# Kernel tuning notes

Hardware: AMD Instinct MI355X
Metric: run time of the kernel (lower is better)

## Reference

```python
import jax, jax.numpy as jnp
import numpy as np

N, NPER, B, E = 65536, 1024, 64, 1048576
IN_F, HID, K, NCLS = 128, 64, 16, 10


def setup_inputs() -> dict:
    key = jax.random.key(0)
    ks = jax.random.split(key, 12)
    x = jax.random.normal(ks[0], (N, IN_F), jnp.float32)
    # block-structured intra-graph edges: 64 graphs of 1024 contiguous nodes
    gid = jax.random.randint(ks[1], (E,), 0, B)
    src = gid * NPER + jax.random.randint(ks[2], (E,), 0, NPER)
    dst = gid * NPER + jax.random.randint(ks[3], (E,), 0, NPER)
    edge_index = jnp.stack([src, dst]).astype(jnp.int32)
    batch = (jnp.arange(N, dtype=jnp.int32) // NPER).astype(jnp.int32)
    def lin(k, fo, fi):
        kw, kb = jax.random.split(k)
        s = 1.0 / np.sqrt(fi)
        return (jax.random.uniform(kw, (fo, fi), jnp.float32, -s, s),
                jax.random.uniform(kb, (fo,), jnp.float32, -s, s))
    W1, b1 = lin(ks[4], HID, IN_F)
    W2, b2 = lin(ks[5], HID, HID)
    Wp, bp = lin(ks[6], K, HID)      # DMoN cluster-assignment MLP (single Linear)
    Wl, bl = lin(ks[7], NCLS, HID)   # final classifier
    return {"x": x, "edge_index": edge_index, "batch": batch,
            "W1": W1, "b1": b1, "W2": W2, "b2": b2,
            "Wp": Wp, "bp": bp, "Wl": Wl, "bl": bl}


def gcn_conv(x, src, dst, W, b):
    # GCNConv with add_self_loops=True, symmetric normalization
    n = x.shape[0]
    deg = jax.ops.segment_sum(jnp.ones(src.shape[0], x.dtype), dst,
                              num_segments=n) + 1.0  # +1 for self-loop
    dinv = jax.lax.rsqrt(deg)
    h = x @ W.T
    coef = (dinv[src] * dinv[dst])[:, None]
    agg = jax.ops.segment_sum(h[src] * coef, dst, num_segments=n)
    agg = agg + h * (dinv * dinv)[:, None]  # self-loop contribution
    return agg + b


def reference(x, edge_index, batch, W1, b1, W2, b2, Wp, bp, Wl, bl):
    src, dst = edge_index[0], edge_index[1]
    h = jax.nn.relu(gcn_conv(x, src, dst, W1, b1))
    h = jax.nn.relu(gcn_conv(h, src, dst, W2, b2))
    # to_dense_batch: graphs are equal-sized and contiguous -> reshape, mask all True
    Xb = h.reshape(B, NPER, HID)
    # DMoN cluster assignment (dropout=0.0, mask all ones)
    s = jax.nn.softmax(Xb @ Wp.T + bp, axis=-1)          # [B, NPER, K]
    Xp = jax.nn.selu(jnp.einsum('bnk,bnh->bkh', s, Xb))   # pooled clusters [B, K, HID]
    out = Xp.mean(axis=1)                                  # [B, HID]
    logits = out @ Wl.T + bl                               # [B, NCLS]
    return logits
```

## Files before the change

kernel.cpp:

```cpp
#include <hip/hip_runtime.h>
#include <cstddef>

#define N_NODES 65536
#define NPER    1024
#define NGRAPH  64
#define HID     64
#define IN_F    128
#define KCLUS   16
#define NCLS    10
#define ECAP    20480
#define HSTRIDE 12
#define ZROW    NPER

__global__ __launch_bounds__(256) void bucket_kernel(const int* __restrict__ src,
                                                     const int* __restrict__ dst,
                                                     int* __restrict__ ecnt,
                                                     int* __restrict__ gedges, int E) {
    __shared__ int hist[NGRAPH];
    __shared__ int base_l[NGRAPH];
    const int t = threadIdx.x;
    const int e0 = blockIdx.x * 1024;
    if (t < NGRAPH) hist[t] = 0;
    __syncthreads();

    int gg[4], rr[4], pk[4];
#pragma unroll
    for (int i = 0; i < 4; ++i) {
        int idx = e0 + i * 256 + t;
        if (idx < E) {
            int d = dst[idx], s = src[idx];
            int g = d >> 10;
            gg[i] = g;
            pk[i] = ((d & 1023) << 10) | (s & 1023);
            rr[i] = atomicAdd(&hist[g], 1);
        } else gg[i] = -1;
    }
    __syncthreads();
    if (t < NGRAPH) base_l[t] = atomicAdd(&ecnt[t], hist[t]);
    __syncthreads();
#pragma unroll
    for (int i = 0; i < 4; ++i) {
        if (gg[i] >= 0) {
            int pos = base_l[gg[i]] + rr[i];
            if (pos < ECAP) gedges[gg[i] * ECAP + pos] = pk[i];
        }
    }
}

__global__ __launch_bounds__(1024) void csr_kernel(const int* __restrict__ gedges,
                                                   const int* __restrict__ ecnt,
                                                   int* __restrict__ rp,
                                                   unsigned short* __restrict__ esorted,
                                                   float* __restrict__ dinv) {
    __shared__ int hist[NPER];
    __shared__ int wsum[16];
    const int g = blockIdx.x, t = threadIdx.x;
    const int lane = t & 63, wid = t >> 6;
    const int ec = ecnt[g];
    const int* ge = gedges + (size_t)g * ECAP;

    hist[t] = 0;
    __syncthreads();
    for (int i = t; i < ec; i += 1024) atomicAdd(&hist[ge[i] >> 10], 1);
    __syncthreads();

    const int h0 = hist[t];
    const int pd = (h0 + 3) & ~3;
    int v = pd;
#pragma unroll
    for (int off = 1; off < 64; off <<= 1) {
        int x = __shfl_up(v, off, 64);
        if (lane >= off) v += x;
    }
    if (lane == 63) wsum[wid] = v;
    __syncthreads();
    if (wid == 0) {
        int wv = (lane < 16) ? wsum[lane] : 0;
#pragma unroll
        for (int off = 1; off < 16; off <<= 1) {
            int x = __shfl_up(wv, off, 64);
            if (lane >= off) wv += x;
        }
        if (lane < 16) wsum[lane] = wv;
    }
    __syncthreads();
    const int incl = v + (wid > 0 ? wsum[wid - 1] : 0);
    const int excl = incl - pd;

    rp[g * (NPER + 1) + t] = excl;
    if (t == NPER - 1) rp[g * (NPER + 1) + NPER] = incl;
    dinv[g * NPER + t] = rsqrtf((float)h0 + 1.0f);

    hist[t] = excl;
    __syncthreads();

    unsigned short* es = esorted + (size_t)g * ECAP;
    for (int i = t; i < ec; i += 1024) {
        int pk = ge[i];
        int pos = atomicAdd(&hist[pk >> 10], 1);
        es[pos] = (unsigned short)(pk & 1023);
    }
    __syncthreads();
    for (int q = excl + h0; q < excl + pd; ++q) es[q] = (unsigned short)ZROW;
}

template <int K>
__global__ __launch_bounds__(256) void linear_kernel(const float* __restrict__ X,
                                                     const float* __restrict__ W,
                                                     float* __restrict__ Y) {
    __shared__ float xsT[64][68];
    __shared__ float wsT[64][68];
    const int t = threadIdx.x;
    const size_t row0 = (size_t)blockIdx.x * 64;
    const int r0 = (t >> 4) * 4;
    const int c0 = (t & 15) * 4;
    float acc[4][4] = {};

    for (int kc = 0; kc < K; kc += 64) {
        __syncthreads();
        for (int i = t; i < 1024; i += 256) {
            int row = i >> 4, k4 = (i & 15) << 2;
            float4 v = *(const float4*)(X + (row0 + row) * K + kc + k4);
            xsT[k4 + 0][row] = v.x;
            xsT[k4 + 1][row] = v.y;
            xsT[k4 + 2][row] = v.z;
            xsT[k4 + 3][row] = v.w;
        }
        for (int i = t; i < 1024; i += 256) {
            int col = i >> 4, k4 = (i & 15) << 2;
            float4 v = *(const float4*)(W + col * K + kc + k4);
            wsT[k4 + 0][col] = v.x;
            wsT[k4 + 1][col] = v.y;
            wsT[k4 + 2][col] = v.z;
            wsT[k4 + 3][col] = v.w;
        }
        __syncthreads();

#pragma unroll 8
        for (int k = 0; k < 64; ++k) {
            float4 xv = *(const float4*)&xsT[k][r0];
            float4 wv = *(const float4*)&wsT[k][c0];
            acc[0][0] = fmaf(xv.x, wv.x, acc[0][0]);
            acc[0][1] = fmaf(xv.x, wv.y, acc[0][1]);
            acc[0][2] = fmaf(xv.x, wv.z, acc[0][2]);
            acc[0][3] = fmaf(xv.x, wv.w, acc[0][3]);
            acc[1][0] = fmaf(xv.y, wv.x, acc[1][0]);
            acc[1][1] = fmaf(xv.y, wv.y, acc[1][1]);
            acc[1][2] = fmaf(xv.y, wv.z, acc[1][2]);
            acc[1][3] = fmaf(xv.y, wv.w, acc[1][3]);
            acc[2][0] = fmaf(xv.z, wv.x, acc[2][0]);
            acc[2][1] = fmaf(xv.z, wv.y, acc[2][1]);
            acc[2][2] = fmaf(xv.z, wv.z, acc[2][2]);
            acc[2][3] = fmaf(xv.z, wv.w, acc[2][3]);
            acc[3][0] = fmaf(xv.w, wv.x, acc[3][0]);
            acc[3][1] = fmaf(xv.w, wv.y, acc[3][1]);
            acc[3][2] = fmaf(xv.w, wv.z, acc[3][2]);
            acc[3][3] = fmaf(xv.w, wv.w, acc[3][3]);
        }
    }

#pragma unroll
    for (int i = 0; i < 4; ++i) {
        float4 v = make_float4(acc[i][0], acc[i][1], acc[i][2], acc[i][3]);
        *(float4*)(Y + (row0 + r0 + i) * HID + c0) = v;
    }
}

__global__ __launch_bounds__(512) void agg_kernel(const float* __restrict__ h,
                                                  const unsigned short* __restrict__ esorted,
                                                  const int* __restrict__ rp,
                                                  const float* __restrict__ dinv,
                                                  const float* __restrict__ bias,
                                                  float* __restrict__ outp) {
    __shared__ float Hs[(NPER + 1) * HSTRIDE];
    __shared__ float dl[NPER];
    const int g = blockIdx.x & 63;
    const int f0 = (blockIdx.x >> 6) * 8;
    const int t = threadIdx.x;
    const int base = g * NPER;

    for (int r = t; r < NPER; r += 512) {
        const float* hp = h + (size_t)(base + r) * HID + f0;
        float4 a = *(const float4*)hp;
        float4 b = *(const float4*)(hp + 4);
        float dv = dinv[base + r];
        dl[r] = dv;
        float* row = &Hs[r * HSTRIDE];
        *(float4*)row = make_float4(a.x * dv, a.y * dv, a.z * dv, a.w * dv);
        *(float4*)(row + 4) = make_float4(b.x * dv, b.y * dv, b.z * dv, b.w * dv);
    }
    if (t < HSTRIDE) Hs[ZROW * HSTRIDE + t] = 0.f;
    float bb[8];
#pragma unroll
    for (int j = 0; j < 8; ++j) bb[j] = bias[f0 + j];
    const unsigned short* es = esorted + (size_t)g * ECAP;
    const int* rpg = rp + g * (NPER + 1);
    __syncthreads();

    for (int ld = t; ld < NPER; ld += 512) {
        int p = rpg[ld];
        const int pe = rpg[ld + 1];
        const float* srow = &Hs[ld * HSTRIDE];
        float4 acc0 = *(const float4*)srow;
        float4 acc1 = *(const float4*)(srow + 4);
        float4 bcc0 = make_float4(0.f, 0.f, 0.f, 0.f);
        float4 bcc1 = make_float4(0.f, 0.f, 0.f, 0.f);

        for (; p < pe; p += 4) {
            uint2 w4 = *(const uint2*)(es + p);
            const float* r0 = &Hs[(int)(w4.x & 0xFFFFu) * HSTRIDE];
            const float* r1 = &Hs[(int)(w4.x >> 16) * HSTRIDE];
            const float* r2 = &Hs[(int)(w4.y & 0xFFFFu) * HSTRIDE];
            const float* r3 = &Hs[(int)(w4.y >> 16) * HSTRIDE];
            float4 a0 = *(const float4*)r0, a1 = *(const float4*)(r0 + 4);
            float4 b0 = *(const float4*)r1, b1 = *(const float4*)(r1 + 4);
            float4 c0v = *(const float4*)r2, c1v = *(const float4*)(r2 + 4);
            float4 d0 = *(const float4*)r3, d1 = *(const float4*)(r3 + 4);
            acc0.x += a0.x; acc0.y += a0.y; acc0.z += a0.z; acc0.w += a0.w;
            acc1.x += a1.x; acc1.y += a1.y; acc1.z += a1.z; acc1.w += a1.w;
            bcc0.x += b0.x; bcc0.y += b0.y; bcc0.z += b0.z; bcc0.w += b0.w;
            bcc1.x += b1.x; bcc1.y += b1.y; bcc1.z += b1.z; bcc1.w += b1.w;
            acc0.x += c0v.x; acc0.y += c0v.y; acc0.z += c0v.z; acc0.w += c0v.w;
            acc1.x += c1v.x; acc1.y += c1v.y; acc1.z += c1v.z; acc1.w += c1v.w;
            bcc0.x += d0.x; bcc0.y += d0.y; bcc0.z += d0.z; bcc0.w += d0.w;
            bcc1.x += d1.x; bcc1.y += d1.y; bcc1.z += d1.z; bcc1.w += d1.w;
        }
        acc0.x += bcc0.x; acc0.y += bcc0.y; acc0.z += bcc0.z; acc0.w += bcc0.w;
        acc1.x += bcc1.x; acc1.y += bcc1.y; acc1.z += bcc1.z; acc1.w += bcc1.w;

        const float dv = dl[ld];
        float4 o0, o1;
        o0.x = fmaxf(fmaf(acc0.x, dv, bb[0]), 0.f);
        o0.y = fmaxf(fmaf(acc0.y, dv, bb[1]), 0.f);
        o0.z = fmaxf(fmaf(acc0.z, dv, bb[2]), 0.f);
        o0.w = fmaxf(fmaf(acc0.w, dv, bb[3]), 0.f);
        o1.x = fmaxf(fmaf(acc1.x, dv, bb[4]), 0.f);
        o1.y = fmaxf(fmaf(acc1.y, dv, bb[5]), 0.f);
        o1.z = fmaxf(fmaf(acc1.z, dv, bb[6]), 0.f);
        o1.w = fmaxf(fmaf(acc1.w, dv, bb[7]), 0.f);
        float* op = outp + (size_t)(base + ld) * HID + f0;
        *(float4*)op = o0;
        *(float4*)(op + 4) = o1;
    }
}

__global__ __launch_bounds__(256) void pool1_kernel(const float* __restrict__ h,
                                                    const float* __restrict__ Wp,
                                                    const float* __restrict__ bp,
                                                    float* __restrict__ xpart) {
    __shared__ float xs[128][HID + 1];
    __shared__ float ss[128][KCLUS + 1];
    __shared__ float wp[KCLUS][HID];
    __shared__ float bps[KCLUS];
    const int g = blockIdx.x >> 3;
    const int c = blockIdx.x & 7;
    const int t = threadIdx.x;
    const float* hb = h + ((size_t)g * NPER + c * 128) * HID;

    for (int i = t; i < 128 * HID / 4; i += 256) {
        float4 v = ((const float4*)hb)[i];
        int row = i >> 4, col = (i & 15) * 4;
        xs[row][col] = v.x; xs[row][col + 1] = v.y; xs[row][col + 2] = v.z; xs[row][col + 3] = v.w;
    }
    for (int i = t; i < KCLUS * HID; i += 256) wp[i >> 6][i & 63] = Wp[i];
    if (t < KCLUS) bps[t] = bp[t];
    __syncthreads();

    if (t < 128) {
        float lg[KCLUS];
        float mx = -1e30f;
#pragma unroll
        for (int k = 0; k < KCLUS; ++k) {
            float a = bps[k];
#pragma unroll 8
            for (int hh = 0; hh < HID; ++hh) a = fmaf(xs[t][hh], wp[k][hh], a);
            lg[k] = a;
            mx = fmaxf(mx, a);
        }
        float sum = 0.f;
#pragma unroll
        for (int k = 0; k < KCLUS; ++k) {
            lg[k] = __expf(lg[k] - mx);
            sum += lg[k];
        }
        float inv = 1.0f / sum;
#pragma unroll
        for (int k = 0; k < KCLUS; ++k) ss[t][k] = lg[k] * inv;
    }
    __syncthreads();

    const int hcol = t & 63;
    const int k0 = (t >> 6) * 4;
    float a0 = 0.f, a1 = 0.f, a2 = 0.f, a3 = 0.f;
#pragma unroll 8
    for (int n = 0; n < 128; ++n) {
        float xv = xs[n][hcol];
        a0 = fmaf(ss[n][k0 + 0], xv, a0);
        a1 = fmaf(ss[n][k0 + 1], xv, a1);
        a2 = fmaf(ss[n][k0 + 2], xv, a2);
        a3 = fmaf(ss[n][k0 + 3], xv, a3);
    }
    float* xp = xpart + (((size_t)(g * 8 + c)) * KCLUS + k0) * HID + hcol;
    xp[0] = a0; xp[HID] = a1; xp[2 * HID] = a2; xp[3 * HID] = a3;
}

__global__ __launch_bounds__(256) void pool2_kernel(const float* __restrict__ xpart,
                                                    const float* __restrict__ Wl,
                                                    const float* __restrict__ bl,
                                                    float* __restrict__ out) {
    __shared__ float xp[KCLUS][HID + 1];
    __shared__ float outm[HID];
    const int g = blockIdx.x;
    const int t = threadIdx.x;
    const int hcol = t & 63;
    const int k0 = (t >> 6) * 4;
    const float* base = xpart + (size_t)g * 8 * KCLUS * HID;

    float a[4] = {};
#pragma unroll
    for (int c = 0; c < 8; ++c)
#pragma unroll
        for (int j = 0; j < 4; ++j)
            a[j] += base[(c * KCLUS + k0 + j) * HID + hcol];

    const float sc = 1.0507009873554805f, al = 1.6732632423543772f;
#pragma unroll
    for (int j = 0; j < 4; ++j) {
        float v = a[j];
        xp[k0 + j][hcol] = v > 0.f ? sc * v : sc * al * (__expf(v) - 1.f);
    }
    __syncthreads();

    if (t < HID) {
        float m = 0.f;
#pragma unroll
        for (int k = 0; k < KCLUS; ++k) m += xp[k][t];
        outm[t] = m * (1.0f / KCLUS);
    }
    __syncthreads();

    if (t < NCLS) {
        float acc = bl[t];
#pragma unroll 8
        for (int hh = 0; hh < HID; ++hh) acc = fmaf(outm[hh], Wl[t * HID + hh], acc);
        out[g * NCLS + t] = acc;
    }
}

extern "C" void kernel_launch(void* const* d_in, const int* in_sizes, int n_in,
                              void* d_out, int out_size, void* d_ws, size_t ws_size,
                              hipStream_t stream) {
    const float* x  = (const float*)d_in[0];
    const int* eidx = (const int*)d_in[1];
    const float* W1 = (const float*)d_in[3];
    const float* b1 = (const float*)d_in[4];
    const float* W2 = (const float*)d_in[5];
    const float* b2 = (const float*)d_in[6];
    const float* Wp = (const float*)d_in[7];
    const float* bp = (const float*)d_in[8];
    const float* Wl = (const float*)d_in[9];
    const float* bl = (const float*)d_in[10];
    float* out = (float*)d_out;

    const int E = in_sizes[1] / 2;
    const int* src = eidx;
    const int* dst = eidx + E;

    char* w = (char*)d_ws;
    int*            ecnt    = (int*)w;            w += 256;
    int*            gedges  = (int*)w;            w += (size_t)NGRAPH * ECAP * 4;
    unsigned short* esorted = (unsigned short*)w; w += (size_t)NGRAPH * ECAP * 2;
    int*            rp      = (int*)w;            w += (size_t)NGRAPH * (NPER + 1) * 4;
    float*          dinv    = (float*)w;          w += (size_t)N_NODES * 4;
    float*          A       = (float*)w;          w += (size_t)N_NODES * HID * 4;
    float*          Bf      = (float*)w;          w += (size_t)N_NODES * HID * 4;
    float*          xpart   = (float*)w;          w += (size_t)NGRAPH * 8 * KCLUS * HID * 4;

    hipMemsetAsync(ecnt, 0, 256, stream);
    bucket_kernel<<<(E + 1023) / 1024, 256, 0, stream>>>(src, dst, ecnt, gedges, E);
    csr_kernel<<<NGRAPH, 1024, 0, stream>>>(gedges, ecnt, rp, esorted, dinv);

    linear_kernel<IN_F><<<N_NODES / 64, 256, 0, stream>>>(x, W1, A);
    agg_kernel<<<NGRAPH * 8, 512, 0, stream>>>(A, esorted, rp, dinv, b1, Bf);

    linear_kernel<HID><<<N_NODES / 64, 256, 0, stream>>>(Bf, W2, A);
    agg_kernel<<<NGRAPH * 8, 512, 0, stream>>>(A, esorted, rp, dinv, b2, Bf);

    pool1_kernel<<<NGRAPH * 8, 256, 0, stream>>>(Bf, Wp, bp, xpart);
    pool2_kernel<<<NGRAPH, 256, 0, stream>>>(xpart, Wl, bl, out);
}
```

Baseline: 230.6 us.

## Fuse GCN linear transform into aggregation kernel per feature slice

Replaces the separate tiled GEMM and aggregation kernels with one conv kernel. Each block computes its 8-column slice of X·W^T directly into shared memory before the sparse aggregation. This removes the intermediate global buffer write/read and two launches. The trade-off is that the input rows are re-read by all 8 feature-slice blocks per graph, with uncoalesced per-thread row reads and no GEMM tiling.

```diff
diff --git a/kernel.cpp b/kernel.cpp
--- a/kernel.cpp
+++ b/kernel.cpp
@@ -105,94 +105,62 @@
 }
 
 template <int K>
-__global__ __launch_bounds__(256) void linear_kernel(const float* __restrict__ X,
-                                                     const float* __restrict__ W,
-                                                     float* __restrict__ Y) {
-    __shared__ float xsT[64][68];
-    __shared__ float wsT[64][68];
-    const int t = threadIdx.x;
-    const size_t row0 = (size_t)blockIdx.x * 64;
-    const int r0 = (t >> 4) * 4;
-    const int c0 = (t & 15) * 4;
-    float acc[4][4] = {};
-
-    for (int kc = 0; kc < K; kc += 64) {
-        __syncthreads();
-        for (int i = t; i < 1024; i += 256) {
-            int row = i >> 4, k4 = (i & 15) << 2;
-            float4 v = *(const float4*)(X + (row0 + row) * K + kc + k4);
-            xsT[k4 + 0][row] = v.x;
-            xsT[k4 + 1][row] = v.y;
-            xsT[k4 + 2][row] = v.z;
-            xsT[k4 + 3][row] = v.w;
-        }
-        for (int i = t; i < 1024; i += 256) {
-            int col = i >> 4, k4 = (i & 15) << 2;
-            float4 v = *(const float4*)(W + col * K + kc + k4);
-            wsT[k4 + 0][col] = v.x;
-            wsT[k4 + 1][col] = v.y;
-            wsT[k4 + 2][col] = v.z;
-            wsT[k4 + 3][col] = v.w;
-        }
-        __syncthreads();
-
-#pragma unroll 8
-        for (int k = 0; k < 64; ++k) {
-            float4 xv = *(const float4*)&xsT[k][r0];
-            float4 wv = *(const float4*)&wsT[k][c0];
-            acc[0][0] = fmaf(xv.x, wv.x, acc[0][0]);
-            acc[0][1] = fmaf(xv.x, wv.y, acc[0][1]);
-            acc[0][2] = fmaf(xv.x, wv.z, acc[0][2]);
-            acc[0][3] = fmaf(xv.x, wv.w, acc[0][3]);
-            acc[1][0] = fmaf(xv.y, wv.x, acc[1][0]);
-            acc[1][1] = fmaf(xv.y, wv.y, acc[1][1]);
-            acc[1][2] = fmaf(xv.y, wv.z, acc[1][2]);
-            acc[1][3] = fmaf(xv.y, wv.w, acc[1][3]);
-            acc[2][0] = fmaf(xv.z, wv.x, acc[2][0]);
-            acc[2][1] = fmaf(xv.z, wv.y, acc[2][1]);
-            acc[2][2] = fmaf(xv.z, wv.z, acc[2][2]);
-            acc[2][3] = fmaf(xv.z, wv.w, acc[2][3]);
-            acc[3][0] = fmaf(xv.w, wv.x, acc[3][0]);
-            acc[3][1] = fmaf(xv.w, wv.y, acc[3][1]);
-            acc[3][2] = fmaf(xv.w, wv.z, acc[3][2]);
-            acc[3][3] = fmaf(xv.w, wv.w, acc[3][3]);
-        }
-    }
-
-#pragma unroll
-    for (int i = 0; i < 4; ++i) {
-        float4 v = make_float4(acc[i][0], acc[i][1], acc[i][2], acc[i][3]);
-        *(float4*)(Y + (row0 + r0 + i) * HID + c0) = v;
-    }
-}
-
-__global__ __launch_bounds__(512) void agg_kernel(const float* __restrict__ h,
-                                                  const unsigned short* __restrict__ esorted,
-                                                  const int* __restrict__ rp,
-                                                  const float* __restrict__ dinv,
-                                                  const float* __restrict__ bias,
-                                                  float* __restrict__ outp) {
+__global__ __launch_bounds__(512) void conv_kernel(const float* __restrict__ X,
+                                                   const float* __restrict__ W,
+                                                   const float* __restrict__ bias,
+                                                   const unsigned short* __restrict__ esorted,
+                                                   const int* __restrict__ rp,
+                                                   const float* __restrict__ dinv,
+                                                   float* __restrict__ outp) {
     __shared__ float Hs[(NPER + 1) * HSTRIDE];
     __shared__ float dl[NPER];
+    __shared__ float wsl[K][8];
     const int g = blockIdx.x & 63;
     const int f0 = (blockIdx.x >> 6) * 8;
     const int t = threadIdx.x;
     const int base = g * NPER;
 
-    for (int r = t; r < NPER; r += 512) {
-        const float* hp = h + (size_t)(base + r) * HID + f0;
-        float4 a = *(const float4*)hp;
-        float4 b = *(const float4*)(hp + 4);
-        float dv = dinv[base + r];
-        dl[r] = dv;
-        float* row = &Hs[r * HSTRIDE];
-        *(float4*)row = make_float4(a.x * dv, a.y * dv, a.z * dv, a.w * dv);
-        *(float4*)(row + 4) = make_float4(b.x * dv, b.y * dv, b.z * dv, b.w * dv);
+    for (int i = t; i < K * 8; i += 512) {
+        int c = i & 7, k = i >> 3;
+        wsl[k][c] = W[(f0 + c) * K + k];
     }
     if (t < HSTRIDE) Hs[ZROW * HSTRIDE + t] = 0.f;
     float bb[8];
 #pragma unroll
     for (int j = 0; j < 8; ++j) bb[j] = bias[f0 + j];
+    __syncthreads();
+
+    {
+        float acc0[8] = {}, acc1[8] = {};
+        const float* x0 = X + (size_t)(base + t) * K;
+        const float* x1 = X + (size_t)(base + t + 512) * K;
+        for (int k4 = 0; k4 < K; k4 += 4) {
+            float4 xa = *(const float4*)(x0 + k4);
+            float4 xb = *(const float4*)(x1 + k4);
+#pragma unroll
+            for (int kk = 0; kk < 4; ++kk) {
+                float xs0 = (kk == 0) ? xa.x : (kk == 1) ? xa.y : (kk == 2) ? xa.z : xa.w;
+                float xs1 = (kk == 0) ? xb.x : (kk == 1) ? xb.y : (kk == 2) ? xb.z : xb.w;
+                const float* wr = wsl[k4 + kk];
+#pragma unroll
+                for (int c = 0; c < 8; ++c) {
+                    float wv = wr[c];
+                    acc0[c] = fmaf(xs0, wv, acc0[c]);
+                    acc1[c] = fmaf(xs1, wv, acc1[c]);
+                }
+            }
+        }
+        float dv0 = dinv[base + t];
+        float dv1 = dinv[base + t + 512];
+        dl[t] = dv0;
+        dl[t + 512] = dv1;
+        float* r0 = &Hs[t * HSTRIDE];
+        float* r1 = &Hs[(t + 512) * HSTRIDE];
+        *(float4*)r0       = make_float4(acc0[0] * dv0, acc0[1] * dv0, acc0[2] * dv0, acc0[3] * dv0);
+        *(float4*)(r0 + 4) = make_float4(acc0[4] * dv0, acc0[5] * dv0, acc0[6] * dv0, acc0[7] * dv0);
+        *(float4*)r1       = make_float4(acc1[0] * dv1, acc1[1] * dv1, acc1[2] * dv1, acc1[3] * dv1);
+        *(float4*)(r1 + 4) = make_float4(acc1[4] * dv1, acc1[5] * dv1, acc1[6] * dv1, acc1[7] * dv1);
+    }
     const unsigned short* es = esorted + (size_t)g * ECAP;
     const int* rpg = rp + g * (NPER + 1);
     __syncthreads();
@@ -372,20 +340,17 @@
     unsigned short* esorted = (unsigned short*)w; w += (size_t)NGRAPH * ECAP * 2;
     int*            rp      = (int*)w;            w += (size_t)NGRAPH * (NPER + 1) * 4;
     float*          dinv    = (float*)w;          w += (size_t)N_NODES * 4;
-    float*          A       = (float*)w;          w += (size_t)N_NODES * HID * 4;
-    float*          Bf      = (float*)w;          w += (size_t)N_NODES * HID * 4;
+    float*          H1      = (float*)w;          w += (size_t)N_NODES * HID * 4;
+    float*          H2      = (float*)w;          w += (size_t)N_NODES * HID * 4;
     float*          xpart   = (float*)w;          w += (size_t)NGRAPH * 8 * KCLUS * HID * 4;
 
     hipMemsetAsync(ecnt, 0, 256, stream);
     bucket_kernel<<<(E + 1023) / 1024, 256, 0, stream>>>(src, dst, ecnt, gedges, E);
     csr_kernel<<<NGRAPH, 1024, 0, stream>>>(gedges, ecnt, rp, esorted, dinv);
 
-    linear_kernel<IN_F><<<N_NODES / 64, 256, 0, stream>>>(x, W1, A);
-    agg_kernel<<<NGRAPH * 8, 512, 0, stream>>>(A, esorted, rp, dinv, b1, Bf);
-
-    linear_kernel<HID><<<N_NODES / 64, 256, 0, stream>>>(Bf, W2, A);
-    agg_kernel<<<NGRAPH * 8, 512, 0, stream>>>(A, esorted, rp, dinv, b2, Bf);
-
-    pool1_kernel<<<NGRAPH * 8, 256, 0, stream>>>(Bf, Wp, bp, xpart);
+    conv_kernel<IN_F><<<NGRAPH * 8, 512, 0, stream>>>(x, W1, b1, esorted, rp, dinv, H1);
+    conv_kernel<HID><<<NGRAPH * 8, 512, 0, stream>>>(H1, W2, b2, esorted, rp, dinv, H2);
+
+    pool1_kernel<<<NGRAPH * 8, 256, 0, stream>>>(H2, Wp, bp, xpart);
     pool2_kernel<<<NGRAPH, 256, 0, stream>>>(xpart, Wl, bl, out);
 }
```

Result: slower. 238.7 us (+3.5%).

## Merge edge bucketing and first linear layer into one heterogeneous launch

Applied to the files above, without the earlier changes.

The edge-bucketing kernel and the first dense linear layer (x @ W1) are combined into a single launch. The first 1024 blocks run the GEMM and the rest bucket edges, reusing the shared memory. The two phases are independent, so they can overlap on the GPU and one launch boundary disappears. The cost is a larger, branchy kernel whose shared-memory footprint applies to the bucketing blocks too, which may lower their occupancy.

```diff
diff --git a/kernel.cpp b/kernel.cpp
--- a/kernel.cpp
+++ b/kernel.cpp
@@ -11,116 +11,61 @@
 #define ECAP    20480
 #define HSTRIDE 12
 #define ZROW    NPER
-
-__global__ __launch_bounds__(256) void bucket_kernel(const int* __restrict__ src,
-                                                     const int* __restrict__ dst,
-                                                     int* __restrict__ ecnt,
-                                                     int* __restrict__ gedges, int E) {
-    __shared__ int hist[NGRAPH];
-    __shared__ int base_l[NGRAPH];
-    const int t = threadIdx.x;
-    const int e0 = blockIdx.x * 1024;
-    if (t < NGRAPH) hist[t] = 0;
-    __syncthreads();
-
-    int gg[4], rr[4], pk[4];
-#pragma unroll
-    for (int i = 0; i < 4; ++i) {
-        int idx = e0 + i * 256 + t;
-        if (idx < E) {
-            int d = dst[idx], s = src[idx];
-            int g = d >> 10;
-            gg[i] = g;
-            pk[i] = ((d & 1023) << 10) | (s & 1023);
-            rr[i] = atomicAdd(&hist[g], 1);
-        } else gg[i] = -1;
-    }
-    __syncthreads();
-    if (t < NGRAPH) base_l[t] = atomicAdd(&ecnt[t], hist[t]);
-    __syncthreads();
-#pragma unroll
-    for (int i = 0; i < 4; ++i) {
-        if (gg[i] >= 0) {
-            int pos = base_l[gg[i]] + rr[i];
-            if (pos < ECAP) gedges[gg[i] * ECAP + pos] = pk[i];
-        }
-    }
-}
-
-__global__ __launch_bounds__(1024) void csr_kernel(const int* __restrict__ gedges,
-                                                   const int* __restrict__ ecnt,
-                                                   int* __restrict__ rp,
-                                                   unsigned short* __restrict__ esorted,
-                                                   float* __restrict__ dinv) {
-    __shared__ int hist[NPER];
-    __shared__ int wsum[16];
-    const int g = blockIdx.x, t = threadIdx.x;
-    const int lane = t & 63, wid = t >> 6;
-    const int ec = ecnt[g];
-    const int* ge = gedges + (size_t)g * ECAP;
-
-    hist[t] = 0;
-    __syncthreads();
-    for (int i = t; i < ec; i += 1024) atomicAdd(&hist[ge[i] >> 10], 1);
-    __syncthreads();
-
-    const int h0 = hist[t];
-    const int pd = (h0 + 3) & ~3;
-    int v = pd;
-#pragma unroll
-    for (int off = 1; off < 64; off <<= 1) {
-        int x = __shfl_up(v, off, 64);
-        if (lane >= off) v += x;
-    }
-    if (lane == 63) wsum[wid] = v;
-    __syncthreads();
-    if (wid == 0) {
-        int wv = (lane < 16) ? wsum[lane] : 0;
-#pragma unroll
-        for (int off = 1; off < 16; off <<= 1) {
-            int x = __shfl_up(wv, off, 64);
-            if (lane >= off) wv += x;
-        }
-        if (lane < 16) wsum[lane] = wv;
-    }
-    __syncthreads();
-    const int incl = v + (wid > 0 ? wsum[wid - 1] : 0);
-    const int excl = incl - pd;
-
-    rp[g * (NPER + 1) + t] = excl;
-    if (t == NPER - 1) rp[g * (NPER + 1) + NPER] = incl;
-    dinv[g * NPER + t] = rsqrtf((float)h0 + 1.0f);
-
-    hist[t] = excl;
-    __syncthreads();
-
-    unsigned short* es = esorted + (size_t)g * ECAP;
-    for (int i = t; i < ec; i += 1024) {
-        int pk = ge[i];
-        int pos = atomicAdd(&hist[pk >> 10], 1);
-        es[pos] = (unsigned short)(pk & 1023);
-    }
-    __syncthreads();
-    for (int q = excl + h0; q < excl + pd; ++q) es[q] = (unsigned short)ZROW;
-}
-
-template <int K>
-__global__ __launch_bounds__(256) void linear_kernel(const float* __restrict__ X,
-                                                     const float* __restrict__ W,
-                                                     float* __restrict__ Y) {
+#define LIN_BLOCKS 1024
+
+__global__ __launch_bounds__(256) void front_kernel(const float* __restrict__ X,
+                                                    const float* __restrict__ W,
+                                                    float* __restrict__ Y,
+                                                    const int* __restrict__ src,
+                                                    const int* __restrict__ dst,
+                                                    int* __restrict__ ecnt,
+                                                    int* __restrict__ gedges, int E) {
     __shared__ float xsT[64][68];
     __shared__ float wsT[64][68];
     const int t = threadIdx.x;
+
+    if (blockIdx.x >= LIN_BLOCKS) {
+        int* hist = (int*)&xsT[0][0];
+        int* base_l = hist + NGRAPH;
+        const int e0 = (blockIdx.x - LIN_BLOCKS) * 1024;
+        if (t < NGRAPH) hist[t] = 0;
+        __syncthreads();
+
+        int gg[4], rr[4], pk[4];
+#pragma unroll
+        for (int i = 0; i < 4; ++i) {
+            int idx = e0 + i * 256 + t;
+            if (idx < E) {
+                int d = dst[idx], s = src[idx];
+                int g = d >> 10;
+                gg[i] = g;
+                pk[i] = ((d & 1023) << 10) | (s & 1023);
+                rr[i] = atomicAdd(&hist[g], 1);
+            } else gg[i] = -1;
+        }
+        __syncthreads();
+        if (t < NGRAPH) base_l[t] = atomicAdd(&ecnt[t], hist[t]);
+        __syncthreads();
+#pragma unroll
+        for (int i = 0; i < 4; ++i) {
+            if (gg[i] >= 0) {
+                int pos = base_l[gg[i]] + rr[i];
+                if (pos < ECAP) gedges[gg[i] * ECAP + pos] = pk[i];
+            }
+        }
+        return;
+    }
+
     const size_t row0 = (size_t)blockIdx.x * 64;
     const int r0 = (t >> 4) * 4;
     const int c0 = (t & 15) * 4;
     float acc[4][4] = {};
 
-    for (int kc = 0; kc < K; kc += 64) {
+    for (int kc = 0; kc < IN_F; kc += 64) {
         __syncthreads();
         for (int i = t; i < 1024; i += 256) {
             int row = i >> 4, k4 = (i & 15) << 2;
-            float4 v = *(const float4*)(X + (row0 + row) * K + kc + k4);
+            float4 v = *(const float4*)(X + (row0 + row) * IN_F + kc + k4);
             xsT[k4 + 0][row] = v.x;
             xsT[k4 + 1][row] = v.y;
             xsT[k4 + 2][row] = v.z;
@@ -128,7 +73,7 @@
         }
         for (int i = t; i < 1024; i += 256) {
             int col = i >> 4, k4 = (i & 15) << 2;
-            float4 v = *(const float4*)(W + col * K + kc + k4);
+            float4 v = *(const float4*)(W + col * IN_F + kc + k4);
             wsT[k4 + 0][col] = v.x;
             wsT[k4 + 1][col] = v.y;
             wsT[k4 + 2][col] = v.z;
@@ -166,6 +111,125 @@
     }
 }
 
+__global__ __launch_bounds__(1024) void csr_kernel(const int* __restrict__ gedges,
+                                                   const int* __restrict__ ecnt,
+                                                   int* __restrict__ rp,
+                                                   unsigned short* __restrict__ esorted,
+                                                   float* __restrict__ dinv) {
+    __shared__ int hist[NPER];
+    __shared__ int wsum[16];
+    const int g = blockIdx.x, t = threadIdx.x;
+    const int lane = t & 63, wid = t >> 6;
+    const int ec = ecnt[g];
+    const int* ge = gedges + (size_t)g * ECAP;
+
+    hist[t] = 0;
+    __syncthreads();
+    for (int i = t; i < ec; i += 1024) atomicAdd(&hist[ge[i] >> 10], 1);
+    __syncthreads();
+
+    const int h0 = hist[t];
+    const int pd = (h0 + 3) & ~3;
+    int v = pd;
+#pragma unroll
+    for (int off = 1; off < 64; off <<= 1) {
+        int x = __shfl_up(v, off, 64);
+        if (lane >= off) v += x;
+    }
+    if (lane == 63) wsum[wid] = v;
+    __syncthreads();
+    if (wid == 0) {
+        int wv = (lane < 16) ? wsum[lane] : 0;
+#pragma unroll
+        for (int off = 1; off < 16; off <<= 1) {
+            int x = __shfl_up(wv, off, 64);
+            if (lane >= off) wv += x;
+        }
+        if (lane < 16) wsum[lane] = wv;
+    }
+    __syncthreads();
+    const int incl = v + (wid > 0 ? wsum[wid - 1] : 0);
+    const int excl = incl - pd;
+
+    rp[g * (NPER + 1) + t] = excl;
+    if (t == NPER - 1) rp[g * (NPER + 1) + NPER] = incl;
+    dinv[g * NPER + t] = rsqrtf((float)h0 + 1.0f);
+
+    hist[t] = excl;
+    __syncthreads();
+
+    unsigned short* es = esorted + (size_t)g * ECAP;
+    for (int i = t; i < ec; i += 1024) {
+        int pk = ge[i];
+        int pos = atomicAdd(&hist[pk >> 10], 1);
+        es[pos] = (unsigned short)(pk & 1023);
+    }
+    __syncthreads();
+    for (int q = excl + h0; q < excl + pd; ++q) es[q] = (unsigned short)ZROW;
+}
+
+template <int K>
+__global__ __launch_bounds__(256) void linear_kernel(const float* __restrict__ X,
+                                                     const float* __restrict__ W,
+                                                     float* __restrict__ Y) {
+    __shared__ float xsT[64][68];
+    __shared__ float wsT[64][68];
+    const int t = threadIdx.x;
+    const size_t row0 = (size_t)blockIdx.x * 64;
+    const int r0 = (t >> 4) * 4;
+    const int c0 = (t & 15) * 4;
+    float acc[4][4] = {};
+
+    for (int kc = 0; kc < K; kc += 64) {
+        __syncthreads();
+        for (int i = t; i < 1024; i += 256) {
+            int row = i >> 4, k4 = (i & 15) << 2;
+            float4 v = *(const float4*)(X + (row0 + row) * K + kc + k4);
+            xsT[k4 + 0][row] = v.x;
+            xsT[k4 + 1][row] = v.y;
+            xsT[k4 + 2][row] = v.z;
+            xsT[k4 + 3][row] = v.w;
+        }
+        for (int i = t; i < 1024; i += 256) {
+            int col = i >> 4, k4 = (i & 15) << 2;
+            float4 v = *(const float4*)(W + col * K + kc + k4);
+            wsT[k4 + 0][col] = v.x;
+            wsT[k4 + 1][col] = v.y;
+            wsT[k4 + 2][col] = v.z;
+            wsT[k4 + 3][col] = v.w;
+        }
+        __syncthreads();
+
+#pragma unroll 8
+        for (int k = 0; k < 64; ++k) {
+            float4 xv = *(const float4*)&xsT[k][r0];
+            float4 wv = *(const float4*)&wsT[k][c0];
+            acc[0][0] = fmaf(xv.x, wv.x, acc[0][0]);
+            acc[0][1] = fmaf(xv.x, wv.y, acc[0][1]);
+            acc[0][2] = fmaf(xv.x, wv.z, acc[0][2]);
+            acc[0][3] = fmaf(xv.x, wv.w, acc[0][3]);
+            acc[1][0] = fmaf(xv.y, wv.x, acc[1][0]);
+            acc[1][1] = fmaf(xv.y, wv.y, acc[1][1]);
+            acc[1][2] = fmaf(xv.y, wv.z, acc[1][2]);
+            acc[1][3] = fmaf(xv.y, wv.w, acc[1][3]);
+            acc[2][0] = fmaf(xv.z, wv.x, acc[2][0]);
+            acc[2][1] = fmaf(xv.z, wv.y, acc[2][1]);
+            acc[2][2] = fmaf(xv.z, wv.z, acc[2][2]);
+            acc[2][3] = fmaf(xv.z, wv.w, acc[2][3]);
+            acc[3][0] = fmaf(xv.w, wv.x, acc[3][0]);
+            acc[3][1] = fmaf(xv.w, wv.y, acc[3][1]);
+            acc[3][2] = fmaf(xv.w, wv.z, acc[3][2]);
+            acc[3][3] = fmaf(xv.w, wv.w, acc[3][3]);
+        }
+    }
+
+#pragma unroll
+    for (int i = 0; i < 4; ++i) {
+        float4 v = make_float4(acc[i][0], acc[i][1], acc[i][2], acc[i][3]);
+        *(float4*)(Y + (row0 + r0 + i) * HID + c0) = v;
+    }
+}
+
 __global__ __launch_bounds__(512) void agg_kernel(const float* __restrict__ h,
                                                   const unsigned short* __restrict__ esorted,
                                                   const int* __restrict__ rp,
@@ -377,10 +441,11 @@
     float*          xpart   = (float*)w;          w += (size_t)NGRAPH * 8 * KCLUS * HID * 4;
 
     hipMemsetAsync(ecnt, 0, 256, stream);
-    bucket_kernel<<<(E + 1023) / 1024, 256, 0, stream>>>(src, dst, ecnt, gedges, E);
+
+    const int nbucket = (E + 1023) / 1024;
+    front_kernel<<<LIN_BLOCKS + nbucket, 256, 0, stream>>>(x, W1, A, src, dst, ecnt, gedges, E);
     csr_kernel<<<NGRAPH, 1024, 0, stream>>>(gedges, ecnt, rp, esorted, dinv);
 
-    linear_kernel<IN_F><<<N_NODES / 64, 256, 0, stream>>>(x, W1, A);
     agg_kernel<<<NGRAPH * 8, 512, 0, stream>>>(A, esorted, rp, dinv, b1, Bf);
 
     linear_kernel<HID><<<N_NODES / 64, 256, 0, stream>>>(Bf, W2, A);
```

Result: faster. 220.9 us (-4.2%).

## Merge edge bucketing with first GEMM in one launch and retile linear kernel

Applied to the files above, without the earlier changes.

Combines the edge-bucketing kernel and the first linear layer into a single heterogeneous launch: the first 512 blocks compute 128-row GEMM tiles and the remaining blocks bucket edges. The goal is to overlap the memory-bound bucketing with the GEMM and save one launch. The GEMM tile also changes from 64x64 with a transposed shared layout to 128x64 with row-major shared tiles, so each thread computes a 4x8 output and reads dot-product style float4 loads. This raises shared memory use and register pressure, which may reduce occupancy, and the output stores become scalar.

```diff
diff --git a/kernel.cpp b/kernel.cpp
--- a/kernel.cpp
+++ b/kernel.cpp
@@ -11,40 +11,110 @@
 #define ECAP    20480
 #define HSTRIDE 12
 #define ZROW    NPER
-
-__global__ __launch_bounds__(256) void bucket_kernel(const int* __restrict__ src,
-                                                     const int* __restrict__ dst,
-                                                     int* __restrict__ ecnt,
-                                                     int* __restrict__ gedges, int E) {
-    __shared__ int hist[NGRAPH];
-    __shared__ int base_l[NGRAPH];
+#define LIN_BLOCKS 512
+
+template <int K>
+__device__ __forceinline__ void gemm_tile(const float* __restrict__ X,
+                                          const float* __restrict__ W,
+                                          float* __restrict__ Y,
+                                          float (*xs)[68], float (*ws)[68],
+                                          int block, int t) {
+    const size_t row0 = (size_t)block * 128;
+    const int rbase = t >> 3;
+    const int cbase = t & 7;
+    float acc[4][8] = {};
+
+    for (int kc = 0; kc < K; kc += 64) {
+        __syncthreads();
+        for (int i = t; i < 128 * 16; i += 256) {
+            int row = i >> 4, k4 = (i & 15) << 2;
+            *(float4*)&xs[row][k4] = *(const float4*)(X + (row0 + row) * K + kc + k4);
+        }
+        for (int i = t; i < 64 * 16; i += 256) {
+            int col = i >> 4, k4 = (i & 15) << 2;
+            *(float4*)&ws[col][k4] = *(const float4*)(W + col * K + kc + k4);
+        }
+        __syncthreads();
+
+#pragma unroll 4
+        for (int k4 = 0; k4 < 64; k4 += 4) {
+            float4 xr[4], wr[8];
+#pragma unroll
+            for (int rr = 0; rr < 4; ++rr) xr[rr] = *(const float4*)&xs[rbase + 32 * rr][k4];
+#pragma unroll
+            for (int cc = 0; cc < 8; ++cc) wr[cc] = *(const float4*)&ws[cbase + 8 * cc][k4];
+#pragma unroll
+            for (int rr = 0; rr < 4; ++rr)
+#pragma unroll
+                for (int cc = 0; cc < 8; ++cc) {
+                    acc[rr][cc] = fmaf(xr[rr].x, wr[cc].x, acc[rr][cc]);
+                    acc[rr][cc] = fmaf(xr[rr].y, wr[cc].y, acc[rr][cc]);
+                    acc[rr][cc] = fmaf(xr[rr].z, wr[cc].z, acc[rr][cc]);
+                    acc[rr][cc] = fmaf(xr[rr].w, wr[cc].w, acc[rr][cc]);
+                }
+        }
+    }
+
+#pragma unroll
+    for (int rr = 0; rr < 4; ++rr)
+#pragma unroll
+        for (int cc = 0; cc < 8; ++cc)
+            Y[(row0 + rbase + 32 * rr) * HID + cbase + 8 * cc] = acc[rr][cc];
+}
+
+__global__ __launch_bounds__(256) void front_kernel(const float* __restrict__ X,
+                                                    const float* __restrict__ W,
+                                                    float* __restrict__ Y,
+                                                    const int* __restrict__ src,
+                                                    const int* __restrict__ dst,
+                                                    int* __restrict__ ecnt,
+                                                    int* __restrict__ gedges, int E) {
+    __shared__ float xs[128][68];
+    __shared__ float ws[64][68];
     const int t = threadIdx.x;
-    const int e0 = blockIdx.x * 1024;
-    if (t < NGRAPH) hist[t] = 0;
-    __syncthreads();
-
-    int gg[4], rr[4], pk[4];
-#pragma unroll
-    for (int i = 0; i < 4; ++i) {
-        int idx = e0 + i * 256 + t;
-        if (idx < E) {
-            int d = dst[idx], s = src[idx];
-            int g = d >> 10;
-            gg[i] = g;
-            pk[i] = ((d & 1023) << 10) | (s & 1023);
-            rr[i] = atomicAdd(&hist[g], 1);
-        } else gg[i] = -1;
-    }
-    __syncthreads();
-    if (t < NGRAPH) base_l[t] = atomicAdd(&ecnt[t], hist[t]);
-    __syncthreads();
-#pragma unroll
-    for (int i = 0; i < 4; ++i) {
-        if (gg[i] >= 0) {
-            int pos = base_l[gg[i]] + rr[i];
-            if (pos < ECAP) gedges[gg[i] * ECAP + pos] = pk[i];
-        }
-    }
+
+    if (blockIdx.x >= LIN_BLOCKS) {
+        int* hist = (int*)&xs[0][0];
+        int* base_l = hist + NGRAPH;
+        const int e0 = (blockIdx.x - LIN_BLOCKS) * 1024;
+        if (t < NGRAPH) hist[t] = 0;
+        __syncthreads();
+
+        int gg[4], rr[4], pk[4];
+#pragma unroll
+        for (int i = 0; i < 4; ++i) {
+            int idx = e0 + i * 256 + t;
+            if (idx < E) {
+                int d = dst[idx], s = src[idx];
+                int g = d >> 10;
+                gg[i] = g;
+                pk[i] = ((d & 1023) << 10) | (s & 1023);
+                rr[i] = atomicAdd(&hist[g], 1);
+            } else gg[i] = -1;
+        }
+        __syncthreads();
+        if (t < NGRAPH) base_l[t] = atomicAdd(&ecnt[t], hist[t]);
+        __syncthreads();
+#pragma unroll
+        for (int i = 0; i < 4; ++i) {
+            if (gg[i] >= 0) {
+                int pos = base_l[gg[i]] + rr[i];
+                if (pos < ECAP) gedges[gg[i] * ECAP + pos] = pk[i];
+            }
+        }
+        return;
+    }
+
+    gemm_tile<IN_F>(X, W, Y, xs, ws, blockIdx.x, t);
+}
+
+template <int K>
+__global__ __launch_bounds__(256) void linear_kernel(const float* __restrict__ X,
+                                                     const float* __restrict__ W,
+                                                     float* __restrict__ Y) {
+    __shared__ float xs[128][68];
+    __shared__ float ws[64][68];
+    gemm_tile<K>(X, W, Y, xs, ws, blockIdx.x, threadIdx.x);
 }
 
 __global__ __launch_bounds__(1024) void csr_kernel(const int* __restrict__ gedges,
@@ -102,68 +172,6 @@
     }
     __syncthreads();
     for (int q = excl + h0; q < excl + pd; ++q) es[q] = (unsigned short)ZROW;
-}
-
-template <int K>
-__global__ __launch_bounds__(256) void linear_kernel(const float* __restrict__ X,
-                                                     const float* __restrict__ W,
-                                                     float* __restrict__ Y) {
-    __shared__ float xsT[64][68];
-    __shared__ float wsT[64][68];
-    const int t = threadIdx.x;
-    const size_t row0 = (size_t)blockIdx.x * 64;
-    const int r0 = (t >> 4) * 4;
-    const int c0 = (t & 15) * 4;
-    float acc[4][4] = {};
-
-    for (int kc = 0; kc < K; kc += 64) {
-        __syncthreads();
-        for (int i = t; i < 1024; i += 256) {
-            int row = i >> 4, k4 = (i & 15) << 2;
-            float4 v = *(const float4*)(X + (row0 + row) * K + kc + k4);
-            xsT[k4 + 0][row] = v.x;
-            xsT[k4 + 1][row] = v.y;
-            xsT[k4 + 2][row] = v.z;
-            xsT[k4 + 3][row] = v.w;
-        }
-        for (int i = t; i < 1024; i += 256) {
-            int col = i >> 4, k4 = (i & 15) << 2;
-            float4 v = *(const float4*)(W + col * K + kc + k4);
-            wsT[k4 + 0][col] = v.x;
-            wsT[k4 + 1][col] = v.y;
-            wsT[k4 + 2][col] = v.z;
-            wsT[k4 + 3][col] = v.w;
-        }
-        __syncthreads();
-
-#pragma unroll 8
-        for (int k = 0; k < 64; ++k) {
-            float4 xv = *(const float4*)&xsT[k][r0];
-            float4 wv = *(const float4*)&wsT[k][c0];
-            acc[0][0] = fmaf(xv.x, wv.x, acc[0][0]);
-            acc[0][1] = fmaf(xv.x, wv.y, acc[0][1]);
-            acc[0][2] = fmaf(xv.x, wv.z, acc[0][2]);
-            acc[0][3] = fmaf(xv.x, wv.w, acc[0][3]);
-            acc[1][0] = fmaf(xv.y, wv.x, acc[1][0]);
-            acc[1][1] = fmaf(xv.y, wv.y, acc[1][1]);
-            acc[1][2] = fmaf(xv.y, wv.z, acc[1][2]);
-            acc[1][3] = fmaf(xv.y, wv.w, acc[1][3]);
-            acc[2][0] = fmaf(xv.z, wv.x, acc[2][0]);
-            acc[2][1] = fmaf(xv.z, wv.y, acc[2][1]);
-            acc[2][2] = fmaf(xv.z, wv.z, acc[2][2]);
-            acc[2][3] = fmaf(xv.z, wv.w, acc[2][3]);
-            acc[3][0] = fmaf(xv.w, wv.x, acc[3][0]);
-            acc[3][1] = fmaf(xv.w, wv.y, acc[3][1]);
-            acc[3][2] = fmaf(xv.w, wv.z, acc[3][2]);
-            acc[3][3] = fmaf(xv.w, wv.w, acc[3][3]);
-        }
-    }
-
-#pragma unroll
-    for (int i = 0; i < 4; ++i) {
-        float4 v = make_float4(acc[i][0], acc[i][1], acc[i][2], acc[i][3]);
-        *(float4*)(Y + (row0 + r0 + i) * HID + c0) = v;
-    }
 }
 
 __global__ __launch_bounds__(512) void agg_kernel(const float* __restrict__ h,
@@ -377,13 +385,14 @@
     float*          xpart   = (float*)w;          w += (size_t)NGRAPH * 8 * KCLUS * HID * 4;
 
     hipMemsetAsync(ecnt, 0, 256, stream);
-    bucket_kernel<<<(E + 1023) / 1024, 256, 0, stream>>>(src, dst, ecnt, gedges, E);
+
+    const int nbucket = (E + 1023) / 1024;
+    front_kernel<<<LIN_BLOCKS + nbucket, 256, 0, stream>>>(x, W1, A, src, dst, ecnt, gedges, E);
     csr_kernel<<<NGRAPH, 1024, 0, stream>>>(gedges, ecnt, rp, esorted, dinv);
 
-    linear_kernel<IN_F><<<N_NODES / 64, 256, 0, stream>>>(x, W1, A);
     agg_kernel<<<NGRAPH * 8, 512, 0, stream>>>(A, esorted, rp, dinv, b1, Bf);
 
-    linear_kernel<HID><<<N_NODES / 64, 256, 0, stream>>>(Bf, W2, A);
+    linear_kernel<HID><<<N_NODES / 128, 256, 0, stream>>>(Bf, W2, A);
     agg_kernel<<<NGRAPH * 8, 512, 0, stream>>>(A, esorted, rp, dinv, b2, Bf);
 
     pool1_kernel<<<NGRAPH * 8, 256, 0, stream>>>(Bf, Wp, bp, xpart);
```

Result: faster. 216.6 us (median of 2 runs) (-6.1%).
